# Kernel optimization log

Measured on AMD Instinct MI355X. Metric: run time of the kernel, lower is better.

Reference implementation:

```python
import jax, jax.numpy as jnp
import numpy as np

B = 4096          # batch
F = 1024          # feature_count * embedding_dim
E = 16            # embedding_dim (domain embedding)
D = 8             # num_domains
T = F + E         # cross-net total dim
L = 3             # cross layers
EPS = 1e-5


def setup_inputs() -> dict:
    key = jax.random.key(0)
    ks = jax.random.split(key, 32)
    s = 0.02
    inp = {}
    inp["x"] = jax.random.normal(ks[0], (B, F), dtype=jnp.float32)
    inp["domain_ids"] = jax.random.randint(ks[1], (B,), 0, D)
    # partitioned normalization params
    inp["pn_weight"] = jnp.ones((D, F), jnp.float32)
    inp["pn_bias"] = jnp.zeros((D, F), jnp.float32)
    # domain embedding table
    inp["dom_emb"] = jax.random.normal(ks[2], (D, E), jnp.float32) * 0.1
    # cross network: L layers, each Linear(T->1, no bias) + additive bias vector
    inp["cross_w"] = jax.random.normal(ks[3], (L, T), jnp.float32) * s
    inp["cross_b"] = jnp.zeros((L, T), jnp.float32)
    # center MLP: T->512->256->128 (ReLU, ReLU, none)
    inp["cW1"] = jax.random.normal(ks[4], (T, 512), jnp.float32) * s
    inp["cb1"] = jnp.zeros((512,), jnp.float32)
    inp["cW2"] = jax.random.normal(ks[5], (512, 256), jnp.float32) * s
    inp["cb2"] = jnp.zeros((256,), jnp.float32)
    inp["cW3"] = jax.random.normal(ks[6], (256, 128), jnp.float32) * s
    inp["cb3"] = jnp.zeros((128,), jnp.float32)
    # per-domain nets: T->512->256->128; last bias initialized to domain_net_init_bias=1.0
    inp["dW1"] = jax.random.normal(ks[7], (D, T, 512), jnp.float32) * s
    inp["db1"] = jnp.zeros((D, 512), jnp.float32)
    inp["dW2"] = jax.random.normal(ks[8], (D, 512, 256), jnp.float32) * s
    inp["db2"] = jnp.zeros((D, 256), jnp.float32)
    inp["dW3"] = jax.random.normal(ks[9], (D, 256, 128), jnp.float32) * s
    inp["db3"] = jnp.ones((D, 128), jnp.float32)
    # final MLP: 128->64->1
    inp["fW1"] = jax.random.normal(ks[10], (128, 64), jnp.float32) * s
    inp["fb1"] = jnp.zeros((64,), jnp.float32)
    inp["fW2"] = jax.random.normal(ks[11], (64, 1), jnp.float32) * s
    inp["fb2"] = jnp.zeros((1,), jnp.float32)
    # auxiliary net: E->32->1
    inp["aW1"] = jax.random.normal(ks[12], (E, 32), jnp.float32) * s
    inp["ab1"] = jnp.zeros((32,), jnp.float32)
    inp["aW2"] = jax.random.normal(ks[13], (32, 1), jnp.float32) * s
    inp["ab2"] = jnp.zeros((1,), jnp.float32)
    return inp


def _forward(x, domain_ids, pn_weight, pn_bias, dom_emb, cross_w, cross_b,
             cW1, cb1, cW2, cb2, cW3, cb3,
             dW1, db1, dW2, db2, dW3, db3,
             fW1, fb1, fW2, fb2, aW1, ab1, aW2, ab2):
    # --- PartitionedNormalization: per-sample LayerNorm stats + domain-indexed affine ---
    mean = jnp.mean(x, axis=1, keepdims=True)
    var = jnp.mean((x - mean) ** 2, axis=1, keepdims=True)  # unbiased=False
    normed = (x - mean) / jnp.sqrt(var + EPS)
    normed = normed * pn_weight[domain_ids] + pn_bias[domain_ids]

    xd = dom_emb[domain_ids]                    # (B, E)
    x0 = jnp.concatenate([normed, xd], axis=1)  # (B, T)

    # --- CrossNetworkWithDomain ---
    xc = x0
    for i in range(L):
        proj = xc @ cross_w[i]                  # (B,)
        xc = x0 * proj[:, None] + cross_b[i] + xc

    # --- center MLP ---
    h = jax.nn.relu(xc @ cW1 + cb1)
    h = jax.nn.relu(h @ cW2 + cb2)
    h_center = h @ cW3 + cb3                    # (B, 128)

    # --- domain-specific nets: run all D nets, select per-sample ---
    a = jax.nn.relu(jnp.einsum('bi,dio->bdo', xc, dW1) + db1[None])   # (B, D, 512)
    a = jax.nn.relu(jnp.einsum('bdi,dio->bdo', a, dW2) + db2[None])   # (B, D, 256)
    a = jnp.einsum('bdi,dio->bdo', a, dW3) + db3[None]                # (B, D, 128)
    h_domain = a[jnp.arange(a.shape[0]), domain_ids]                  # (B, 128)

    # --- STAR fusion (tanh) ---
    fused = h_center * jnp.tanh(h_domain)

    # --- final MLP + auxiliary net ---
    main_logits = jax.nn.relu(fused @ fW1 + fb1) @ fW2 + fb2          # (B, 1)
    aux_logits = jax.nn.relu(xd @ aW1 + ab1) @ aW2 + ab2              # (B, 1)
    return jax.nn.sigmoid(main_logits + aux_logits)


def reference(x, domain_ids, pn_weight, pn_bias, dom_emb, cross_w, cross_b,
              cW1, cb1, cW2, cb2, cW3, cb3,
              dW1, db1, dW2, db2, dW3, db3,
              fW1, fb1, fW2, fb2, aW1, ab1, aW2, ab2):
    return _forward(x, domain_ids, pn_weight, pn_bias, dom_emb, cross_w, cross_b,
                    cW1, cb1, cW2, cb2, cW3, cb3,
                    dW1, db1, dW2, db2, dW3, db3,
                    fW1, fb1, fW2, fb2, aW1, ab1, aW2, ab2)
```

## Files before the change

kernel.cpp:

```cpp
#include <hip/hip_runtime.h>
#include <math.h>
#include <stdint.h>

#define BATCH 4096
#define FEAT  1024
#define EDIM  16
#define NDOM  8
#define TDIM  1040
#define KP1   1088
#define NLAYER 3
#define EPSV  1e-5f

typedef __attribute__((ext_vector_type(8))) short bf16x8;
typedef __attribute__((ext_vector_type(4))) float f32x4;

__device__ __forceinline__ unsigned short f2bf(float f) {
    union { float f; unsigned int u; } v; v.f = f;
    unsigned int u = v.u;
    return (unsigned short)((u + 0x7fffu + ((u >> 16) & 1u)) >> 16);
}
__device__ __forceinline__ float bf2f(unsigned short u) {
    union { unsigned int u; float f; } v; v.u = ((unsigned int)u) << 16; return v.f;
}
__device__ __forceinline__ void gload_lds16(const void* g, void* l) {
    __builtin_amdgcn_global_load_lds(
        (const __attribute__((address_space(1))) void*)(g),
        (__attribute__((address_space(3))) void*)(l), 16, 0, 0);
}

#define T_W1 136
#define T_W2 32
#define T_W3 8
#define NCONV (T_W1*9 + T_W2*9 + T_W3*9)

__global__ __launch_bounds__(256) void front(
    const int* __restrict__ dom, int* __restrict__ perm, int* __restrict__ starts,
    const float* __restrict__ cW1, const float* __restrict__ dW1,
    const float* __restrict__ cW2, const float* __restrict__ dW2,
    const float* __restrict__ cW3, const float* __restrict__ dW3,
    unsigned short* __restrict__ Wc1b, unsigned short* __restrict__ Wd1b,
    unsigned short* __restrict__ Wc2b, unsigned short* __restrict__ Wd2b,
    unsigned short* __restrict__ Wc3b, unsigned short* __restrict__ Wd3b,
    const float* __restrict__ x,
    const float* __restrict__ pnw, const float* __restrict__ pnb,
    const float* __restrict__ demb,
    const float* __restrict__ crw, const float* __restrict__ crb,
    const float* __restrict__ aW1, const float* __restrict__ ab1,
    const float* __restrict__ aW2, const float* __restrict__ ab2,
    unsigned short* __restrict__ XCb, float* __restrict__ auxg) {
    int b = blockIdx.x;
    int t = threadIdx.x;

    if (b < NCONV) {
        __shared__ float tile[64][65];
        const float* src; unsigned short* dst; int K, N, Kp, rr;
        if (b < T_W1)            { src = cW1; dst = Wc1b; K = TDIM; N = 512; Kp = KP1; rr = b; }
        else if (b < T_W1*9)     { int r = b - T_W1; int z = r / T_W1; rr = r % T_W1;
                                   src = dW1 + (size_t)z * TDIM * 512; dst = Wd1b + (size_t)z * 512 * KP1;
                                   K = TDIM; N = 512; Kp = KP1; }
        else if (b < T_W1*9+T_W2)   { src = cW2; dst = Wc2b; K = 512; N = 256; Kp = 512; rr = b - T_W1*9; }
        else if (b < T_W1*9+T_W2*9) { int r = b - (T_W1*9+T_W2); int z = r / T_W2; rr = r % T_W2;
                                   src = dW2 + (size_t)z * 512 * 256; dst = Wd2b + (size_t)z * 256 * 512;
                                   K = 512; N = 256; Kp = 512; }
        else if (b < T_W1*9+T_W2*9+T_W3) { src = cW3; dst = Wc3b; K = 256; N = 128; Kp = 256; rr = b - (T_W1*9+T_W2*9); }
        else                     { int r = b - (T_W1*9+T_W2*9+T_W3); int z = r / T_W3; rr = r % T_W3;
                                   src = dW3 + (size_t)z * 256 * 128; dst = Wd3b + (size_t)z * 128 * 256;
                                   K = 256; N = 128; Kp = 256; }
        int kt = Kp >> 6;
        int kb = rr % kt, nb = rr / kt;
        int k0 = kb * 64, n0 = nb * 64;
        #pragma unroll
        for (int i = 0; i < 4; i++) {
            int flat = t + i * 256;
            int kr = flat >> 4, c4 = flat & 15;
            int k = k0 + kr;
            float4 v = make_float4(0.f, 0.f, 0.f, 0.f);
            if (k < K) v = *(const float4*)(src + (size_t)k * N + n0 + c4 * 4);
            tile[kr][c4 * 4 + 0] = v.x;
            tile[kr][c4 * 4 + 1] = v.y;
            tile[kr][c4 * 4 + 2] = v.z;
            tile[kr][c4 * 4 + 3] = v.w;
        }
        __syncthreads();
        #pragma unroll
        for (int i = 0; i < 4; i++) {
            int flat = t + i * 256;
            int n = flat >> 4, kg = flat & 15;
            ushort4 sv;
            sv.x = f2bf(tile[kg * 4 + 0][n]);
            sv.y = f2bf(tile[kg * 4 + 1][n]);
            sv.z = f2bf(tile[kg * 4 + 2][n]);
            sv.w = f2bf(tile[kg * 4 + 3][n]);
            *(ushort4*)(dst + (size_t)(n0 + n) * Kp + k0 + kg * 4) = sv;
        }
        return;
    }
    if (b == NCONV) {
        __shared__ int cnt[NDOM];
        __shared__ int off[NDOM];
        if (t < NDOM) cnt[t] = 0;
        __syncthreads();
        for (int i = t; i < BATCH; i += 256) atomicAdd(&cnt[dom[i]], 1);
        __syncthreads();
        if (t == 0) {
            int s = 0;
            for (int d = 0; d < NDOM; d++) { off[d] = s; starts[d] = s; s += cnt[d]; }
            starts[NDOM] = s;
        }
        __syncthreads();
        for (int i = t; i < BATCH; i += 256) {
            int p = atomicAdd(&off[dom[i]], 1);
            perm[p] = i;
        }
        return;
    }

    int w = t >> 6, lane = t & 63;
    int row = (b - NCONV - 1) * 4 + w;
    int d = dom[row];

    float4 X[4];
    #pragma unroll
    for (int j = 0; j < 4; j++)
        X[j] = *(const float4*)(x + (size_t)row * FEAT + 4 * lane + 256 * j);

    float s = 0.f, ss = 0.f;
    #pragma unroll
    for (int j = 0; j < 4; j++) {
        s  += X[j].x + X[j].y + X[j].z + X[j].w;
        ss += X[j].x*X[j].x + X[j].y*X[j].y + X[j].z*X[j].z + X[j].w*X[j].w;
    }
    #pragma unroll
    for (int m = 1; m < 64; m <<= 1) {
        s  += __shfl_xor(s,  m);
        ss += __shfl_xor(ss, m);
    }
    float mean = s / (float)FEAT;
    float var  = ss / (float)FEAT - mean * mean;
    float rstd = rsqrtf(var + EPSV);

    float4 x0[4], xc[4];
    #pragma unroll
    for (int j = 0; j < 4; j++) {
        float4 wv = *(const float4*)(pnw + (size_t)d * FEAT + 4 * lane + 256 * j);
        float4 bv = *(const float4*)(pnb + (size_t)d * FEAT + 4 * lane + 256 * j);
        x0[j].x = (X[j].x - mean) * rstd * wv.x + bv.x;
        x0[j].y = (X[j].y - mean) * rstd * wv.y + bv.y;
        x0[j].z = (X[j].z - mean) * rstd * wv.z + bv.z;
        x0[j].w = (X[j].w - mean) * rstd * wv.w + bv.w;
        xc[j] = x0[j];
    }
    float x0e = 0.f, xce = 0.f;
    if (lane < EDIM) { x0e = demb[d * EDIM + lane]; xce = x0e; }

    #pragma unroll
    for (int l = 0; l < NLAYER; l++) {
        const float* wl = crw + l * TDIM;
        const float* bl = crb + l * TDIM;
        float partial = 0.f;
        #pragma unroll
        for (int j = 0; j < 4; j++) {
            float4 wv = *(const float4*)(wl + 4 * lane + 256 * j);
            partial += xc[j].x*wv.x + xc[j].y*wv.y + xc[j].z*wv.z + xc[j].w*wv.w;
        }
        if (lane < EDIM) partial += xce * wl[FEAT + lane];
        #pragma unroll
        for (int m = 1; m < 64; m <<= 1) partial += __shfl_xor(partial, m);
        float proj = partial;
        #pragma unroll
        for (int j = 0; j < 4; j++) {
            float4 bv = *(const float4*)(bl + 4 * lane + 256 * j);
            xc[j].x = fmaf(x0[j].x, proj, bv.x + xc[j].x);
            xc[j].y = fmaf(x0[j].y, proj, bv.y + xc[j].y);
            xc[j].z = fmaf(x0[j].z, proj, bv.z + xc[j].z);
            xc[j].w = fmaf(x0[j].w, proj, bv.w + xc[j].w);
        }
        if (lane < EDIM) xce = fmaf(x0e, proj, bl[FEAT + lane] + xce);
    }

    #pragma unroll
    for (int j = 0; j < 4; j++) {
        ushort4 sv;
        sv.x = f2bf(xc[j].x); sv.y = f2bf(xc[j].y);
        sv.z = f2bf(xc[j].z); sv.w = f2bf(xc[j].w);
        *(ushort4*)(XCb + (size_t)row * KP1 + 4 * lane + 256 * j) = sv;
    }
    XCb[(size_t)row * KP1 + FEAT + lane] = (lane < EDIM) ? f2bf(xce) : 0;

    float h = (lane < 32) ? ab1[lane] : 0.f;
    #pragma unroll
    for (int e = 0; e < EDIM; e++) {
        float ev = __shfl(xce, e);
        if (lane < 32) h = fmaf(ev, aW1[e * 32 + lane], h);
    }
    float c = (lane < 32) ? fmaxf(h, 0.f) * aW2[lane] : 0.f;
    #pragma unroll
    for (int m = 1; m < 64; m <<= 1) c += __shfl_xor(c, m);
    if (lane == 0) auxg[row] = c + ab2[0];
}

__global__ __launch_bounds__(256) void gemm_mfma_v3(
    const unsigned short* __restrict__ Ac, const unsigned short* __restrict__ Ad, int lda,
    const unsigned short* __restrict__ Wc, const unsigned short* __restrict__ Wd,
    const float* __restrict__ bc, const float* __restrict__ bd,
    unsigned short* __restrict__ Cc, unsigned short* __restrict__ Cd,
    const int* __restrict__ starts, const int* __restrict__ perm, int usePerm,
    int Kp, int N, int relu) {
    __shared__ short As[128 * 64];
    __shared__ short Bs[64 * 64];

    const unsigned short* A; const unsigned short* W; const float* bias;
    unsigned short* C;
    int m0, mEnd;
    int y = blockIdx.y;
    if (y < 32) {
        A = Ac; W = Wc; bias = bc; C = Cc;
        m0 = y * 128; mEnd = BATCH;
    } else {
        int yy = y - 32;
        int d = yy >> 5, sl = yy & 31;
        int ds = starts[d], de = starts[d + 1];
        m0 = ds + sl * 128;
        if (m0 >= de) return;
        mEnd = de;
        A = Ad; W = Wd + (size_t)d * N * Kp; bias = bd + d * N; C = Cd;
    }
    int n0 = blockIdx.x * 64;
    int tid = threadIdx.x;
    int w = tid >> 6, lane = tid & 63;
    int wm = w >> 1, wn = w & 1;
    int lr = lane & 15, q = lane >> 4;

    const unsigned short* pA[4]; const unsigned short* pB[2];
    short* dA[4]; short* dB[2];
    #pragma unroll
    for (int i = 0; i < 4; i++) {
        int seg = i * 4 + w;
        int ch = seg * 64 + lane;
        int loc = ch >> 3, c = ch & 7;
        int mm = m0 + loc; if (mm > mEnd - 1) mm = mEnd - 1;
        int rowp = usePerm ? perm[mm] : mm;
        pA[i] = A + (size_t)rowp * lda + ((c ^ (loc & 7)) << 3);
        dA[i] = As + seg * 512;
    }
    #pragma unroll
    for (int i = 0; i < 2; i++) {
        int seg = i * 4 + w;
        int ch = seg * 64 + lane;
        int loc = ch >> 3, c = ch & 7;
        pB[i] = W + (size_t)(n0 + loc) * Kp + ((c ^ (loc & 7)) << 3);
        dB[i] = Bs + seg * 512;
    }

    f32x4 acc[4][2];
    #pragma unroll
    for (int i = 0; i < 4; i++)
        #pragma unroll
        for (int j = 0; j < 2; j++)
            acc[i][j] = (f32x4){0.f, 0.f, 0.f, 0.f};

    for (int k0 = 0; k0 < Kp; k0 += 64) {
        #pragma unroll
        for (int i = 0; i < 4; i++) gload_lds16(pA[i] + k0, dA[i]);
        #pragma unroll
        for (int i = 0; i < 2; i++) gload_lds16(pB[i] + k0, dB[i]);
        __syncthreads();

        #pragma unroll
        for (int half = 0; half < 2; half++) {
            int c = half * 4 + q;
            bf16x8 af[4], bf[2];
            #pragma unroll
            for (int i = 0; i < 4; i++) {
                int m = wm * 64 + i * 16 + lr;
                af[i] = *(const bf16x8*)(As + m * 64 + ((c ^ (m & 7)) << 3));
            }
            #pragma unroll
            for (int j = 0; j < 2; j++) {
                int n = wn * 32 + j * 16 + lr;
                bf[j] = *(const bf16x8*)(Bs + n * 64 + ((c ^ (n & 7)) << 3));
            }
            #pragma unroll
            for (int i = 0; i < 4; i++)
                #pragma unroll
                for (int j = 0; j < 2; j++)
                    acc[i][j] = __builtin_amdgcn_mfma_f32_16x16x32_bf16(
                        af[i], bf[j], acc[i][j], 0, 0, 0);
        }
        __syncthreads();
    }

    #pragma unroll
    for (int i = 0; i < 4; i++) {
        #pragma unroll
        for (int j = 0; j < 2; j++) {
            int col = n0 + wn * 32 + j * 16 + lr;
            float bvv = bias[col];
            int rowb = m0 + wm * 64 + i * 16 + q * 4;
            #pragma unroll
            for (int r = 0; r < 4; r++) {
                int row = rowb + r;
                if (row >= mEnd) continue;
                float val = acc[i][j][r] + bvv;
                if (relu) val = fmaxf(val, 0.f);
                C[(size_t)row * N + col] = f2bf(val);
            }
        }
    }
}

__global__ __launch_bounds__(256) void gemm_mfma_v4(
    const unsigned short* __restrict__ Ac, const unsigned short* __restrict__ Ad, int lda,
    const unsigned short* __restrict__ Wc, const unsigned short* __restrict__ Wd,
    const float* __restrict__ bc, const float* __restrict__ bd,
    unsigned short* __restrict__ Cc, unsigned short* __restrict__ Cd,
    const int* __restrict__ starts,
    int Kp, int N, int relu) {
    __shared__ short As[64 * 64];
    __shared__ short Bs[64 * 64];

    const unsigned short* A; const unsigned short* W; const float* bias;
    unsigned short* C;
    int m0, mEnd;
    int y = blockIdx.y;
    if (y < 64) {
        A = Ac; W = Wc; bias = bc; C = Cc;
        m0 = y * 64; mEnd = BATCH;
    } else {
        int yy = y - 64;
        int d = yy >> 4, sl = yy & 15;
        int ds = starts[d], de = starts[d + 1];
        m0 = ds + sl * 64;
        if (m0 >= de) return;
        mEnd = de;
        A = Ad; W = Wd + (size_t)d * N * Kp; bias = bd + d * N; C = Cd;
    }
    int n0 = blockIdx.x * 64;
    int tid = threadIdx.x;
    int w = tid >> 6, lane = tid & 63;
    int wm = w >> 1, wn = w & 1;
    int lr = lane & 15, q = lane >> 4;

    const unsigned short* pA[2]; const unsigned short* pB[2];
    short* dA[2]; short* dB[2];
    #pragma unroll
    for (int i = 0; i < 2; i++) {
        int seg = i * 4 + w;
        int ch = seg * 64 + lane;
        int loc = ch >> 3, c = ch & 7;
        int mm = m0 + loc; if (mm > mEnd - 1) mm = mEnd - 1;
        pA[i] = A + (size_t)mm * lda + ((c ^ (loc & 7)) << 3);
        dA[i] = As + seg * 512;
        pB[i] = W + (size_t)(n0 + loc) * Kp + ((c ^ (loc & 7)) << 3);
        dB[i] = Bs + seg * 512;
    }

    f32x4 acc[2][2];
    #pragma unroll
    for (int i = 0; i < 2; i++)
        #pragma unroll
        for (int j = 0; j < 2; j++)
            acc[i][j] = (f32x4){0.f, 0.f, 0.f, 0.f};

    for (int k0 = 0; k0 < Kp; k0 += 64) {
        #pragma unroll
        for (int i = 0; i < 2; i++) gload_lds16(pA[i] + k0, dA[i]);
        #pragma unroll
        for (int i = 0; i < 2; i++) gload_lds16(pB[i] + k0, dB[i]);
        __syncthreads();

        #pragma unroll
        for (int half = 0; half < 2; half++) {
            int c = half * 4 + q;
            bf16x8 af[2], bf[2];
            #pragma unroll
            for (int i = 0; i < 2; i++) {
                int m = wm * 32 + i * 16 + lr;
                af[i] = *(const bf16x8*)(As + m * 64 + ((c ^ (m & 7)) << 3));
            }
            #pragma unroll
            for (int j = 0; j < 2; j++) {
                int n = wn * 32 + j * 16 + lr;
                bf[j] = *(const bf16x8*)(Bs + n * 64 + ((c ^ (n & 7)) << 3));
            }
            #pragma unroll
            for (int i = 0; i < 2; i++)
                #pragma unroll
                for (int j = 0; j < 2; j++)
                    acc[i][j] = __builtin_amdgcn_mfma_f32_16x16x32_bf16(
                        af[i], bf[j], acc[i][j], 0, 0, 0);
        }
        __syncthreads();
    }

    #pragma unroll
    for (int i = 0; i < 2; i++) {
        #pragma unroll
        for (int j = 0; j < 2; j++) {
            int col = n0 + wn * 32 + j * 16 + lr;
            float bvv = bias[col];
            int rowb = m0 + wm * 32 + i * 16 + q * 4;
            #pragma unroll
            for (int r = 0; r < 4; r++) {
                int row = rowb + r;
                if (row >= mEnd) continue;
                float val = acc[i][j][r] + bvv;
                if (relu) val = fmaxf(val, 0.f);
                C[(size_t)row * N + col] = f2bf(val);
            }
        }
    }
}

__global__ __launch_bounds__(256) void gemm3_final(
    const unsigned short* __restrict__ Ac, const unsigned short* __restrict__ Ad,
    const unsigned short* __restrict__ Wc, const unsigned short* __restrict__ Wd,
    const float* __restrict__ bc, const float* __restrict__ bd,
    const float* __restrict__ fW1, const float* __restrict__ fb1,
    const float* __restrict__ fW2, const float* __restrict__ fb2,
    const float* __restrict__ auxg, const int* __restrict__ perm,
    const int* __restrict__ starts, float* __restrict__ out) {
    __shared__ __align__(16) char smem[28672];
    short* As    = (short*)smem;
    short* Bs    = (short*)(smem + 4096);
    short* fused = (short*)(smem + 20480);

    int y = blockIdx.x;
    int d = y >> 7, sl = y & 127;
    int ds = starts[d], de = starts[d + 1];
    int m0 = ds + sl * 32;
    if (m0 >= de) return;
    int mEnd = de;

    int tid = threadIdx.x;
    int w = tid >> 6, lane = tid & 63;
    int wm = w >> 1, wn = w & 1;
    int lr = lane & 15, q = lane >> 4;
    const uint4 zero16 = make_uint4(0u, 0u, 0u, 0u);

    for (int chain = 0; chain < 2; chain++) {
        const unsigned short* A = chain ? Ad : Ac;
        const unsigned short* W = chain ? (Wd + (size_t)d * 128 * 256) : Wc;
        const float* bias = chain ? (bd + d * 128) : bc;
        f32x4 acc[4];
        #pragma unroll
        for (int j = 0; j < 4; j++) acc[j] = (f32x4){0.f, 0.f, 0.f, 0.f};

        for (int k0 = 0; k0 < 256; k0 += 64) {
            {
                int m = tid >> 3, c = tid & 7;
                int row = m0 + m;
                uint4 val = (row < mEnd)
                    ? *(const uint4*)(A + (size_t)row * 256 + k0 + c * 8) : zero16;
                *(uint4*)(As + m * 64 + ((c ^ (m & 7)) * 8)) = val;
            }
            #pragma unroll
            for (int i = 0; i < 4; i++) {
                int flat = tid + i * 256;
                int n = flat >> 3, c = flat & 7;
                uint4 val = *(const uint4*)(W + (size_t)n * 256 + k0 + c * 8);
                *(uint4*)(Bs + n * 64 + ((c ^ (n & 7)) * 8)) = val;
            }
            __syncthreads();
            #pragma unroll
            for (int g = 0; g < 2; g++) {
                int c = g * 4 + q;
                int m = wm * 16 + lr;
                bf16x8 af = *(const bf16x8*)(As + m * 64 + ((c ^ (m & 7)) * 8));
                #pragma unroll
                for (int j = 0; j < 4; j++) {
                    int n = wn * 64 + j * 16 + lr;
                    bf16x8 bf = *(const bf16x8*)(Bs + n * 64 + ((c ^ (n & 7)) * 8));
                    acc[j] = __builtin_amdgcn_mfma_f32_16x16x32_bf16(af, bf, acc[j], 0, 0, 0);
                }
            }
            __syncthreads();
        }
        #pragma unroll
        for (int j = 0; j < 4; j++) {
            int col = wn * 64 + j * 16 + lr;
            float bvv = bias[col];
            int cch = col >> 3;
            #pragma unroll
            for (int r = 0; r < 4; r++) {
                int row = wm * 16 + q * 4 + r;
                int pc = (cch & 8) | ((cch ^ (row & 7)) & 7);
                int idx = row * 128 + pc * 8 + (col & 7);
                if (chain == 0) {
                    fused[idx] = (short)f2bf(acc[j][r] + bvv);
                } else {
                    float cv = bf2f((unsigned short)fused[idx]);
                    fused[idx] = (short)f2bf(cv * tanhf(acc[j][r] + bvv));
                }
            }
        }
        __syncthreads();
    }

    short* Bsf = Bs;
    float* Ls  = (float*)As;
    for (int s2 = tid; s2 < 1024; s2 += 256) {
        int n = s2 >> 4, cch = s2 & 15;
        bf16x8 vv;
        #pragma unroll
        for (int kk = 0; kk < 8; kk++)
            vv[kk] = (short)f2bf(fW1[(cch * 8 + kk) * 64 + n]);
        int pc = (cch & 8) | ((cch ^ (n & 7)) & 7);
        *(bf16x8*)(Bsf + n * 128 + pc * 8) = vv;
    }
    __syncthreads();

    f32x4 acc2[2];
    #pragma unroll
    for (int j = 0; j < 2; j++) acc2[j] = (f32x4){0.f, 0.f, 0.f, 0.f};
    #pragma unroll
    for (int g = 0; g < 4; g++) {
        int c = g * 4 + q;
        int m = wm * 16 + lr;
        int pcm = (c & 8) | ((c ^ (m & 7)) & 7);
        bf16x8 af = *(const bf16x8*)(fused + m * 128 + pcm * 8);
        #pragma unroll
        for (int j = 0; j < 2; j++) {
            int n = wn * 32 + j * 16 + lr;
            int pcn = (c & 8) | ((c ^ (n & 7)) & 7);
            bf16x8 bf = *(const bf16x8*)(Bsf + n * 128 + pcn * 8);
            acc2[j] = __builtin_amdgcn_mfma_f32_16x16x32_bf16(af, bf, acc2[j], 0, 0, 0);
        }
    }

    float w2v[2], b1v[2];
    #pragma unroll
    for (int j = 0; j < 2; j++) {
        int col = wn * 32 + j * 16 + lr;
        w2v[j] = fW2[col];
        b1v[j] = fb1[col];
    }
    float rowv[4];
    #pragma unroll
    for (int r = 0; r < 4; r++) {
        float v = 0.f;
        #pragma unroll
        for (int j = 0; j < 2; j++)
            v += fmaxf(acc2[j][r] + b1v[j], 0.f) * w2v[j];
        v += __shfl_xor(v, 1);
        v += __shfl_xor(v, 2);
        v += __shfl_xor(v, 4);
        v += __shfl_xor(v, 8);
        rowv[r] = v;
    }
    if (wn == 0 && lr == 0) {
        #pragma unroll
        for (int r = 0; r < 4; r++)
            Ls[wm * 16 + q * 4 + r] = rowv[r];
    }
    __syncthreads();
    if (wn == 1 && lr == 0) {
        float b2 = fb2[0];
        #pragma unroll
        for (int r = 0; r < 4; r++) {
            int row = wm * 16 + q * 4 + r;
            int p = m0 + row;
            if (p < mEnd) {
                int orow = perm[p];
                float logit = Ls[row] + rowv[r] + b2 + auxg[orow];
                out[orow] = 1.f / (1.f + expf(-logit));
            }
        }
    }
}

extern "C" void kernel_launch(void* const* d_in, const int* in_sizes, int n_in,
                              void* d_out, int out_size, void* d_ws, size_t ws_size,
                              hipStream_t stream) {
    (void)in_sizes; (void)n_in; (void)out_size; (void)ws_size;

    const float* x    = (const float*)d_in[0];
    const int*   dom  = (const int*)  d_in[1];
    const float* pnw  = (const float*)d_in[2];
    const float* pnb  = (const float*)d_in[3];
    const float* demb = (const float*)d_in[4];
    const float* crw  = (const float*)d_in[5];
    const float* crb  = (const float*)d_in[6];
    const float* cW1  = (const float*)d_in[7];
    const float* cb1  = (const float*)d_in[8];
    const float* cW2  = (const float*)d_in[9];
    const float* cb2  = (const float*)d_in[10];
    const float* cW3  = (const float*)d_in[11];
    const float* cb3  = (const float*)d_in[12];
    const float* dW1  = (const float*)d_in[13];
    const float* db1  = (const float*)d_in[14];
    const float* dW2  = (const float*)d_in[15];
    const float* db2  = (const float*)d_in[16];
    const float* dW3  = (const float*)d_in[17];
    const float* db3  = (const float*)d_in[18];
    const float* fW1  = (const float*)d_in[19];
    const float* fb1  = (const float*)d_in[20];
    const float* fW2  = (const float*)d_in[21];
    const float* fb2  = (const float*)d_in[22];
    const float* aW1  = (const float*)d_in[23];
    const float* ab1  = (const float*)d_in[24];
    const float* aW2  = (const float*)d_in[25];
    const float* ab2  = (const float*)d_in[26];
    float* out = (float*)d_out;

    char* base = (char*)d_ws;
    size_t o = 0;
    auto alloc = [&](size_t bytes) { char* p = base + o; o += (bytes + 255) & ~size_t(255); return p; };

    int* perm   = (int*)alloc(BATCH * 4);
    int* starts = (int*)alloc((NDOM + 1) * 4);
    float* auxg = (float*)alloc(BATCH * 4);
    unsigned short* XCb  = (unsigned short*)alloc((size_t)BATCH * KP1 * 2);
    unsigned short* H1c  = (unsigned short*)alloc((size_t)BATCH * 512 * 2);
    unsigned short* H1d  = (unsigned short*)alloc((size_t)BATCH * 512 * 2);
    unsigned short* H2c  = (unsigned short*)alloc((size_t)BATCH * 256 * 2);
    unsigned short* H2d  = (unsigned short*)alloc((size_t)BATCH * 256 * 2);
    unsigned short* Wc1b = (unsigned short*)alloc((size_t)512 * KP1 * 2);
    unsigned short* Wd1b = (unsigned short*)alloc((size_t)NDOM * 512 * KP1 * 2);
    unsigned short* Wc2b = (unsigned short*)alloc((size_t)256 * 512 * 2);
    unsigned short* Wd2b = (unsigned short*)alloc((size_t)NDOM * 256 * 512 * 2);
    unsigned short* Wc3b = (unsigned short*)alloc((size_t)128 * 256 * 2);
    unsigned short* Wd3b = (unsigned short*)alloc((size_t)NDOM * 128 * 256 * 2);

    front<<<NCONV + 1 + BATCH / 4, 256, 0, stream>>>(
        dom, perm, starts, cW1, dW1, cW2, dW2, cW3, dW3,
        Wc1b, Wd1b, Wc2b, Wd2b, Wc3b, Wd3b,
        x, pnw, pnb, demb, crw, crb, aW1, ab1, aW2, ab2, XCb, auxg);

    gemm_mfma_v3<<<dim3(512 / 64, 32 + NDOM * 32), 256, 0, stream>>>(
        XCb, XCb, KP1, Wc1b, Wd1b, cb1, db1, H1c, H1d, starts, perm, 1, KP1, 512, 1);
    gemm_mfma_v4<<<dim3(256 / 64, 64 + NDOM * 16), 256, 0, stream>>>(
        H1c, H1d, 512, Wc2b, Wd2b, cb2, db2, H2c, H2d, starts, 512, 256, 1);

    gemm3_final<<<NDOM * 128, 256, 0, stream>>>(
        H2c, H2d, Wc3b, Wd3b, cb3, db3, fW1, fb1, fW2, fb2,
        auxg, perm, starts, out);
}
```

Measured before the change: 209.7 us.

## Fuse layer-2 GEMM into tail kernel with double-buffered LDS pipeline

Replaces the separate layer-2 GEMM kernel and the layer-3/final kernel with a single tail kernel. Each 32-row block computes H2 for both the center and domain chains directly in LDS, then runs layer 3 and the final MLP, so the H2 global round trip and one launch go away. Weight and activation tiles are double-buffered with async global-to-LDS loads across both stages. The cost is 96KB of LDS per block, which lowers occupancy, and the full 256x512 W2 matrix is re-read from L2 by every 32-row block.

```diff
diff --git a/kernel.cpp b/kernel.cpp
--- a/kernel.cpp
+++ b/kernel.cpp
@@ -309,121 +309,22 @@
     }
 }
 
-__global__ __launch_bounds__(256) void gemm_mfma_v4(
-    const unsigned short* __restrict__ Ac, const unsigned short* __restrict__ Ad, int lda,
-    const unsigned short* __restrict__ Wc, const unsigned short* __restrict__ Wd,
-    const float* __restrict__ bc, const float* __restrict__ bd,
-    unsigned short* __restrict__ Cc, unsigned short* __restrict__ Cd,
-    const int* __restrict__ starts,
-    int Kp, int N, int relu) {
-    __shared__ short As[64 * 64];
-    __shared__ short Bs[64 * 64];
-
-    const unsigned short* A; const unsigned short* W; const float* bias;
-    unsigned short* C;
-    int m0, mEnd;
-    int y = blockIdx.y;
-    if (y < 64) {
-        A = Ac; W = Wc; bias = bc; C = Cc;
-        m0 = y * 64; mEnd = BATCH;
-    } else {
-        int yy = y - 64;
-        int d = yy >> 4, sl = yy & 15;
-        int ds = starts[d], de = starts[d + 1];
-        m0 = ds + sl * 64;
-        if (m0 >= de) return;
-        mEnd = de;
-        A = Ad; W = Wd + (size_t)d * N * Kp; bias = bd + d * N; C = Cd;
-    }
-    int n0 = blockIdx.x * 64;
-    int tid = threadIdx.x;
-    int w = tid >> 6, lane = tid & 63;
-    int wm = w >> 1, wn = w & 1;
-    int lr = lane & 15, q = lane >> 4;
-
-    const unsigned short* pA[2]; const unsigned short* pB[2];
-    short* dA[2]; short* dB[2];
-    #pragma unroll
-    for (int i = 0; i < 2; i++) {
-        int seg = i * 4 + w;
-        int ch = seg * 64 + lane;
-        int loc = ch >> 3, c = ch & 7;
-        int mm = m0 + loc; if (mm > mEnd - 1) mm = mEnd - 1;
-        pA[i] = A + (size_t)mm * lda + ((c ^ (loc & 7)) << 3);
-        dA[i] = As + seg * 512;
-        pB[i] = W + (size_t)(n0 + loc) * Kp + ((c ^ (loc & 7)) << 3);
-        dB[i] = Bs + seg * 512;
-    }
-
-    f32x4 acc[2][2];
-    #pragma unroll
-    for (int i = 0; i < 2; i++)
-        #pragma unroll
-        for (int j = 0; j < 2; j++)
-            acc[i][j] = (f32x4){0.f, 0.f, 0.f, 0.f};
-
-    for (int k0 = 0; k0 < Kp; k0 += 64) {
-        #pragma unroll
-        for (int i = 0; i < 2; i++) gload_lds16(pA[i] + k0, dA[i]);
-        #pragma unroll
-        for (int i = 0; i < 2; i++) gload_lds16(pB[i] + k0, dB[i]);
-        __syncthreads();
-
-        #pragma unroll
-        for (int half = 0; half < 2; half++) {
-            int c = half * 4 + q;
-            bf16x8 af[2], bf[2];
-            #pragma unroll
-            for (int i = 0; i < 2; i++) {
-                int m = wm * 32 + i * 16 + lr;
-                af[i] = *(const bf16x8*)(As + m * 64 + ((c ^ (m & 7)) << 3));
-            }
-            #pragma unroll
-            for (int j = 0; j < 2; j++) {
-                int n = wn * 32 + j * 16 + lr;
-                bf[j] = *(const bf16x8*)(Bs + n * 64 + ((c ^ (n & 7)) << 3));
-            }
-            #pragma unroll
-            for (int i = 0; i < 2; i++)
-                #pragma unroll
-                for (int j = 0; j < 2; j++)
-                    acc[i][j] = __builtin_amdgcn_mfma_f32_16x16x32_bf16(
-                        af[i], bf[j], acc[i][j], 0, 0, 0);
-        }
-        __syncthreads();
-    }
-
-    #pragma unroll
-    for (int i = 0; i < 2; i++) {
-        #pragma unroll
-        for (int j = 0; j < 2; j++) {
-            int col = n0 + wn * 32 + j * 16 + lr;
-            float bvv = bias[col];
-            int rowb = m0 + wm * 32 + i * 16 + q * 4;
-            #pragma unroll
-            for (int r = 0; r < 4; r++) {
-                int row = rowb + r;
-                if (row >= mEnd) continue;
-                float val = acc[i][j][r] + bvv;
-                if (relu) val = fmaxf(val, 0.f);
-                C[(size_t)row * N + col] = f2bf(val);
-            }
-        }
-    }
-}
-
-__global__ __launch_bounds__(256) void gemm3_final(
-    const unsigned short* __restrict__ Ac, const unsigned short* __restrict__ Ad,
-    const unsigned short* __restrict__ Wc, const unsigned short* __restrict__ Wd,
-    const float* __restrict__ bc, const float* __restrict__ bd,
+__global__ __launch_bounds__(256) void tail_fused(
+    const unsigned short* __restrict__ H1c, const unsigned short* __restrict__ H1d,
+    const unsigned short* __restrict__ Wc2, const unsigned short* __restrict__ Wd2,
+    const float* __restrict__ cb2v, const float* __restrict__ db2v,
+    const unsigned short* __restrict__ Wc3, const unsigned short* __restrict__ Wd3,
+    const float* __restrict__ cb3v, const float* __restrict__ db3v,
     const float* __restrict__ fW1, const float* __restrict__ fb1,
     const float* __restrict__ fW2, const float* __restrict__ fb2,
     const float* __restrict__ auxg, const int* __restrict__ perm,
     const int* __restrict__ starts, float* __restrict__ out) {
-    __shared__ __align__(16) char smem[28672];
-    short* As    = (short*)smem;
-    short* Bs    = (short*)(smem + 4096);
-    short* fused = (short*)(smem + 20480);
+
+    __shared__ __align__(16) char smem[98304];
+    short* Bsb[2] = { (short*)smem, (short*)(smem + 32768) };
+    short* Asb[2] = { (short*)(smem + 65536), (short*)(smem + 69632) };
+    short* H2    = (short*)(smem + 73728);
+    short* fused = (short*)(smem + 90112);
 
     int y = blockIdx.x;
     int d = y >> 7, sl = y & 127;
@@ -434,71 +335,159 @@
 
     int tid = threadIdx.x;
     int w = tid >> 6, lane = tid & 63;
-    int wm = w >> 1, wn = w & 1;
     int lr = lane & 15, q = lane >> 4;
-    const uint4 zero16 = make_uint4(0u, 0u, 0u, 0u);
-
-    for (int chain = 0; chain < 2; chain++) {
-        const unsigned short* A = chain ? Ad : Ac;
-        const unsigned short* W = chain ? (Wd + (size_t)d * 128 * 256) : Wc;
-        const float* bias = chain ? (bd + d * 128) : bc;
-        f32x4 acc[4];
-        #pragma unroll
-        for (int j = 0; j < 4; j++) acc[j] = (f32x4){0.f, 0.f, 0.f, 0.f};
-
-        for (int k0 = 0; k0 < 256; k0 += 64) {
-            {
-                int m = tid >> 3, c = tid & 7;
-                int row = m0 + m;
-                uint4 val = (row < mEnd)
-                    ? *(const uint4*)(A + (size_t)row * 256 + k0 + c * 8) : zero16;
-                *(uint4*)(As + m * 64 + ((c ^ (m & 7)) * 8)) = val;
-            }
-            #pragma unroll
-            for (int i = 0; i < 4; i++) {
-                int flat = tid + i * 256;
-                int n = flat >> 3, c = flat & 7;
-                uint4 val = *(const uint4*)(W + (size_t)n * 256 + k0 + c * 8);
-                *(uint4*)(Bs + n * 64 + ((c ^ (n & 7)) * 8)) = val;
+
+    int bn = w * 8 + (lane >> 3);
+    int sw = ((lane & 7) ^ (bn & 7)) << 3;
+    int rowA = m0 + bn; if (rowA > mEnd - 1) rowA = mEnd - 1;
+
+    const unsigned short* pA0  = H1c + (size_t)rowA * 512 + sw;
+    const unsigned short* pA1  = H1d + (size_t)rowA * 512 + sw;
+    const unsigned short* pW20 = Wc2 + (size_t)bn * 512 + sw;
+    const unsigned short* pW21 = Wd2 + (size_t)d * 256 * 512 + (size_t)bn * 512 + sw;
+    const unsigned short* pW30 = Wc3 + (size_t)bn * 256 + sw;
+    const unsigned short* pW31 = Wd3 + (size_t)d * 128 * 256 + (size_t)bn * 256 + sw;
+
+    auto stage_l2 = [&](int c, int k0, int pb) {
+        const unsigned short* pa = c ? pA1 : pA0;
+        const unsigned short* pw = c ? pW21 : pW20;
+        gload_lds16(pa + k0, Asb[pb] + w * 512);
+        #pragma unroll
+        for (int i = 0; i < 8; i++)
+            gload_lds16(pw + (size_t)i * 32 * 512 + k0, Bsb[pb] + (i * 4 + w) * 512);
+    };
+    auto stage_l3 = [&](int c, int k0, int pb) {
+        const unsigned short* pw = c ? pW31 : pW30;
+        #pragma unroll
+        for (int i = 0; i < 4; i++)
+            gload_lds16(pw + (size_t)i * 32 * 256 + k0, Bsb[pb] + (i * 4 + w) * 512);
+    };
+
+    stage_l2(0, 0, 0);
+    __syncthreads();
+
+    #pragma unroll
+    for (int c = 0; c < 2; c++) {
+        f32x4 acc2[2][4];
+        #pragma unroll
+        for (int i = 0; i < 2; i++)
+            #pragma unroll
+            for (int j = 0; j < 4; j++) acc2[i][j] = (f32x4){0.f, 0.f, 0.f, 0.f};
+
+        #pragma unroll
+        for (int it = 0; it < 8; it++) {
+            int t = c * 12 + it;
+            int pb = t & 1, pn = pb ^ 1;
+            if (it < 7) stage_l2(c, (it + 1) * 64, pn);
+            else        stage_l3(c, 0, pn);
+
+            #pragma unroll
+            for (int half = 0; half < 2; half++) {
+                int cc = half * 4 + q;
+                bf16x8 af[2], bf[4];
+                #pragma unroll
+                for (int i = 0; i < 2; i++) {
+                    int m = i * 16 + lr;
+                    af[i] = *(const bf16x8*)(Asb[pb] + m * 64 + ((cc ^ (m & 7)) << 3));
+                }
+                #pragma unroll
+                for (int j = 0; j < 4; j++) {
+                    int n = w * 64 + j * 16 + lr;
+                    bf[j] = *(const bf16x8*)(Bsb[pb] + n * 64 + ((cc ^ (n & 7)) << 3));
+                }
+                #pragma unroll
+                for (int i = 0; i < 2; i++)
+                    #pragma unroll
+                    for (int j = 0; j < 4; j++)
+                        acc2[i][j] = __builtin_amdgcn_mfma_f32_16x16x32_bf16(
+                            af[i], bf[j], acc2[i][j], 0, 0, 0);
             }
             __syncthreads();
-            #pragma unroll
-            for (int g = 0; g < 2; g++) {
-                int c = g * 4 + q;
-                int m = wm * 16 + lr;
-                bf16x8 af = *(const bf16x8*)(As + m * 64 + ((c ^ (m & 7)) * 8));
-                #pragma unroll
-                for (int j = 0; j < 4; j++) {
-                    int n = wn * 64 + j * 16 + lr;
-                    bf16x8 bf = *(const bf16x8*)(Bs + n * 64 + ((c ^ (n & 7)) * 8));
-                    acc[j] = __builtin_amdgcn_mfma_f32_16x16x32_bf16(af, bf, acc[j], 0, 0, 0);
+        }
+
+        const float* b2 = c ? (db2v + d * 256) : cb2v;
+        #pragma unroll
+        for (int i = 0; i < 2; i++)
+            #pragma unroll
+            for (int j = 0; j < 4; j++) {
+                int col = w * 64 + j * 16 + lr;
+                float bv = b2[col];
+                int cch = col >> 3;
+                #pragma unroll
+                for (int r = 0; r < 4; r++) {
+                    int row = i * 16 + q * 4 + r;
+                    int pc = (cch & 24) | ((cch ^ (row & 7)) & 7);
+                    float v = fmaxf(acc2[i][j][r] + bv, 0.f);
+                    H2[row * 256 + pc * 8 + (col & 7)] = (short)f2bf(v);
                 }
             }
+        __syncthreads();
+
+        f32x4 acc3[2][2];
+        #pragma unroll
+        for (int i = 0; i < 2; i++)
+            #pragma unroll
+            for (int j = 0; j < 2; j++) acc3[i][j] = (f32x4){0.f, 0.f, 0.f, 0.f};
+
+        #pragma unroll
+        for (int it = 0; it < 4; it++) {
+            int t = c * 12 + 8 + it;
+            int pb = t & 1, pn = pb ^ 1;
+            if (it < 3)      stage_l3(c, (it + 1) * 64, pn);
+            else if (c == 0) stage_l2(1, 0, pn);
+
+            #pragma unroll
+            for (int half = 0; half < 2; half++) {
+                int cc = half * 4 + q;
+                int C = it * 8 + cc;
+                bf16x8 af[2], bf[2];
+                #pragma unroll
+                for (int i = 0; i < 2; i++) {
+                    int m = i * 16 + lr;
+                    int pcm = (C & 24) | ((C ^ (m & 7)) & 7);
+                    af[i] = *(const bf16x8*)(H2 + m * 256 + pcm * 8);
+                }
+                #pragma unroll
+                for (int j = 0; j < 2; j++) {
+                    int n = w * 32 + j * 16 + lr;
+                    bf[j] = *(const bf16x8*)(Bsb[pb] + n * 64 + ((cc ^ (n & 7)) << 3));
+                }
+                #pragma unroll
+                for (int i = 0; i < 2; i++)
+                    #pragma unroll
+                    for (int j = 0; j < 2; j++)
+                        acc3[i][j] = __builtin_amdgcn_mfma_f32_16x16x32_bf16(
+                            af[i], bf[j], acc3[i][j], 0, 0, 0);
+            }
             __syncthreads();
         }
-        #pragma unroll
-        for (int j = 0; j < 4; j++) {
-            int col = wn * 64 + j * 16 + lr;
-            float bvv = bias[col];
-            int cch = col >> 3;
-            #pragma unroll
-            for (int r = 0; r < 4; r++) {
-                int row = wm * 16 + q * 4 + r;
-                int pc = (cch & 8) | ((cch ^ (row & 7)) & 7);
-                int idx = row * 128 + pc * 8 + (col & 7);
-                if (chain == 0) {
-                    fused[idx] = (short)f2bf(acc[j][r] + bvv);
-                } else {
-                    float cv = bf2f((unsigned short)fused[idx]);
-                    fused[idx] = (short)f2bf(cv * tanhf(acc[j][r] + bvv));
+
+        const float* b3 = c ? (db3v + d * 128) : cb3v;
+        #pragma unroll
+        for (int i = 0; i < 2; i++)
+            #pragma unroll
+            for (int j = 0; j < 2; j++) {
+                int col = w * 32 + j * 16 + lr;
+                float bv = b3[col];
+                int cch = col >> 3;
+                #pragma unroll
+                for (int r = 0; r < 4; r++) {
+                    int row = i * 16 + q * 4 + r;
+                    int pc = (cch & 8) | ((cch ^ (row & 7)) & 7);
+                    int idx = row * 128 + pc * 8 + (col & 7);
+                    if (c == 0) {
+                        fused[idx] = (short)f2bf(acc3[i][j][r] + bv);
+                    } else {
+                        float cv = bf2f((unsigned short)fused[idx]);
+                        fused[idx] = (short)f2bf(cv * tanhf(acc3[i][j][r] + bv));
+                    }
                 }
             }
-        }
-        __syncthreads();
-    }
-
-    short* Bsf = Bs;
-    float* Ls  = (float*)As;
+        __syncthreads();
+    }
+
+    short* Bsf = Bsb[0];
+    float* Ls  = (float*)Asb[0];
     for (int s2 = tid; s2 < 1024; s2 += 256) {
         int n = s2 >> 4, cch = s2 & 15;
         bf16x8 vv;
@@ -510,21 +499,22 @@
     }
     __syncthreads();
 
-    f32x4 acc2[2];
-    #pragma unroll
-    for (int j = 0; j < 2; j++) acc2[j] = (f32x4){0.f, 0.f, 0.f, 0.f};
+    int wm = w >> 1, wn = w & 1;
+    f32x4 acc2f[2];
+    #pragma unroll
+    for (int j = 0; j < 2; j++) acc2f[j] = (f32x4){0.f, 0.f, 0.f, 0.f};
     #pragma unroll
     for (int g = 0; g < 4; g++) {
-        int c = g * 4 + q;
+        int cc = g * 4 + q;
         int m = wm * 16 + lr;
-        int pcm = (c & 8) | ((c ^ (m & 7)) & 7);
+        int pcm = (cc & 8) | ((cc ^ (m & 7)) & 7);
         bf16x8 af = *(const bf16x8*)(fused + m * 128 + pcm * 8);
         #pragma unroll
         for (int j = 0; j < 2; j++) {
             int n = wn * 32 + j * 16 + lr;
-            int pcn = (c & 8) | ((c ^ (n & 7)) & 7);
+            int pcn = (cc & 8) | ((cc ^ (n & 7)) & 7);
             bf16x8 bf = *(const bf16x8*)(Bsf + n * 128 + pcn * 8);
-            acc2[j] = __builtin_amdgcn_mfma_f32_16x16x32_bf16(af, bf, acc2[j], 0, 0, 0);
+            acc2f[j] = __builtin_amdgcn_mfma_f32_16x16x32_bf16(af, bf, acc2f[j], 0, 0, 0);
         }
     }
 
@@ -541,7 +531,7 @@
         float v = 0.f;
         #pragma unroll
         for (int j = 0; j < 2; j++)
-            v += fmaxf(acc2[j][r] + b1v[j], 0.f) * w2v[j];
+            v += fmaxf(acc2f[j][r] + b1v[j], 0.f) * w2v[j];
         v += __shfl_xor(v, 1);
         v += __shfl_xor(v, 2);
         v += __shfl_xor(v, 4);
@@ -613,8 +603,6 @@
     unsigned short* XCb  = (unsigned short*)alloc((size_t)BATCH * KP1 * 2);
     unsigned short* H1c  = (unsigned short*)alloc((size_t)BATCH * 512 * 2);
     unsigned short* H1d  = (unsigned short*)alloc((size_t)BATCH * 512 * 2);
-    unsigned short* H2c  = (unsigned short*)alloc((size_t)BATCH * 256 * 2);
-    unsigned short* H2d  = (unsigned short*)alloc((size_t)BATCH * 256 * 2);
     unsigned short* Wc1b = (unsigned short*)alloc((size_t)512 * KP1 * 2);
     unsigned short* Wd1b = (unsigned short*)alloc((size_t)NDOM * 512 * KP1 * 2);
     unsigned short* Wc2b = (unsigned short*)alloc((size_t)256 * 512 * 2);
@@ -629,10 +617,8 @@
 
     gemm_mfma_v3<<<dim3(512 / 64, 32 + NDOM * 32), 256, 0, stream>>>(
         XCb, XCb, KP1, Wc1b, Wd1b, cb1, db1, H1c, H1d, starts, perm, 1, KP1, 512, 1);
-    gemm_mfma_v4<<<dim3(256 / 64, 64 + NDOM * 16), 256, 0, stream>>>(
-        H1c, H1d, 512, Wc2b, Wd2b, cb2, db2, H2c, H2d, starts, 512, 256, 1);
-
-    gemm3_final<<<NDOM * 128, 256, 0, stream>>>(
-        H2c, H2d, Wc3b, Wd3b, cb3, db3, fW1, fb1, fW2, fb2,
-        auxg, perm, starts, out);
+
+    tail_fused<<<NDOM * 128, 256, 0, stream>>>(
+        H1c, H1d, Wc2b, Wd2b, cb2, db2, Wc3b, Wd3b, cb3, db3,
+        fW1, fb1, fW2, fb2, auxg, perm, starts, out);
 }
```

Result: faster. 197.0 us (-6.0%).
